# Performance work log

Hardware: AMD Instinct MI355X
Metric: run time of the kernel (lower is better)

Reference implementation:

```python
import jax, jax.numpy as jnp
import numpy as np

D_MODEL = 1024
N_HEADS = 16
MAX_SEQ = 1024
BATCH = 4

def _first_primes(n):
    limit = n * 15
    sieve = np.ones(limit, dtype=bool)
    sieve[:2] = False
    for i in range(2, int(limit ** 0.5) + 1):
        if sieve[i]:
            sieve[i * i::i] = False
    return np.flatnonzero(sieve)[:n]

def _pi_attention_bias(n_heads, max_seq_len):
    # bias[h, t, s] = 0.1 * sin(prime[h]*pi * (t - s) / max_seq_len)
    primes = _first_primes(n_heads).astype(np.float32)
    freqs = primes * np.pi  # [H]
    pos = np.arange(max_seq_len, dtype=np.float32)
    pos_diff = pos[:, None] - pos[None, :]  # [T, T]
    bias = np.sin(freqs[:, None, None] * pos_diff[None] / max_seq_len) * 0.1
    return jnp.asarray(bias, dtype=jnp.float32)

def setup_inputs() -> dict:
    key = jax.random.key(0)
    ks = jax.random.split(key, 8)
    D = D_MODEL
    xavier = (6.0 / (D + D)) ** 0.5
    inp = {
        'x': jax.random.normal(ks[0], (BATCH, MAX_SEQ, D), dtype=jnp.float32),
        'Wq': jax.random.uniform(ks[1], (D, D), jnp.float32, -xavier, xavier),
        'bq': jnp.zeros((D,), jnp.float32),
        'Wk': jax.random.uniform(ks[2], (D, D), jnp.float32, -xavier, xavier),
        'bk': jnp.zeros((D,), jnp.float32),
        'Wv': jax.random.uniform(ks[3], (D, D), jnp.float32, -xavier, xavier),
        'bv': jnp.zeros((D,), jnp.float32),
        'Wo': jax.random.uniform(ks[4], (D, D), jnp.float32, -xavier, xavier),
        'bo': jnp.zeros((D,), jnp.float32),
        'pi_bias': _pi_attention_bias(N_HEADS, MAX_SEQ),
        'bias_scale': jnp.asarray(0.1, jnp.float32),
        'spectral_alpha': jnp.asarray(1.0, jnp.float32),
    }
    return inp

def reference(x, Wq, bq, Wk, bk, Wv, bv, Wo, bo, pi_bias, bias_scale, spectral_alpha):
    B, T, D = x.shape
    H = N_HEADS
    hd = D // H
    scale = 1.0 / (hd ** 0.5)

    def split_heads(y):
        return y.reshape(B, T, H, hd).transpose(0, 2, 1, 3)  # [B,H,T,hd]

    q = split_heads(x @ Wq + bq)
    k = split_heads(x @ Wk + bk)
    v = split_heads(x @ Wv + bv)

    # spectral filter along the time axis (use_spectral and T > 4)
    freqs = jnp.fft.fftfreq(T).astype(jnp.float32)  # [T]
    filt = jnp.exp(-jnp.abs(spectral_alpha) * jnp.abs(freqs))[None, None, :, None]
    q = jnp.fft.ifft(jnp.fft.fft(q, axis=2, norm='ortho') * filt, axis=2, norm='ortho').real
    k = jnp.fft.ifft(jnp.fft.fft(k, axis=2, norm='ortho') * filt, axis=2, norm='ortho').real

    scores = jnp.einsum('bhtd,bhsd->bhts', q, k) * scale
    scores = scores + bias_scale * pi_bias[None, :, :T, :T]
    attn = jax.nn.softmax(scores, axis=-1)  # dropout is identity in eval
    out = jnp.einsum('bhts,bhsd->bhtd', attn, v)
    out = out.transpose(0, 2, 1, 3).reshape(B, T, D)
    return out @ Wo + bo
```

## Files before the change

kernel.cpp:

```cpp
#include <hip/hip_runtime.h>
#include <hip/hip_bf16.h>

typedef __bf16 bf16x8 __attribute__((ext_vector_type(8)));
typedef float f32x4 __attribute__((ext_vector_type(4)));

#define OFF_G      0x0ULL
#define OFF_GMAT   0x10000ULL
#define OFF_XB     0x210000ULL
#define OFF_XBT    0xA10000ULL
#define OFF_XF     0x1210000ULL
#define OFF_WQT    0x1A10000ULL
#define OFF_WKT    0x1C10000ULL
#define OFF_WVT    0x1E10000ULL
#define OFF_WOT    0x2010000ULL
#define OFF_KB     0x2210000ULL
#define OFF_VTB    0x2A10000ULL

static __device__ __forceinline__ unsigned short f2bf(float f) {
  union { float f; unsigned int u; } v; v.f = f;
  unsigned int r = v.u + 0x7FFFu + ((v.u >> 16) & 1u);
  return (unsigned short)(r >> 16);
}

static __device__ __forceinline__ void g2l16(const unsigned short* g, unsigned short* l) {
  __builtin_amdgcn_global_load_lds(
      (const __attribute__((address_space(1))) unsigned int*)g,
      (__attribute__((address_space(3))) unsigned int*)l, 16, 0, 0);
}

__constant__ float PRIMES_F[16] = {2.f, 3.f, 5.f, 7.f, 11.f, 13.f, 17.f, 19.f,
                                   23.f, 29.f, 31.f, 37.f, 41.f, 43.f, 47.f, 53.f};

__global__ __launch_bounds__(256) void k_g(const float* __restrict__ alpha_p,
                                           float* __restrict__ g) {
  const int d = blockIdx.x;
  const float alpha = fabsf(alpha_p[0]);
  float partial = 0.f;
  for (int j = threadIdx.x; j < 1024; j += 256) {
    int jm = (j <= 512) ? j : 1024 - j;
    float filt = __expf(-alpha * (float)jm * (1.0f / 1024.f));
    int p = (j * d) & 1023;
    partial += filt * __cosf((float)p * (6.28318530717958647692f / 1024.f));
  }
  __shared__ float red[4];
  #pragma unroll
  for (int off = 32; off > 0; off >>= 1) partial += __shfl_down(partial, off, 64);
  if ((threadIdx.x & 63) == 0) red[threadIdx.x >> 6] = partial;
  __syncthreads();
  if (threadIdx.x == 0) g[d] = (red[0] + red[1] + red[2] + red[3]) * (1.f / 1024.f);
}

__global__ __launch_bounds__(256) void k_gmat(const float* __restrict__ g,
                                              unsigned short* __restrict__ Gm) {
  int i = blockIdx.x * 256 + threadIdx.x;
  int t = i >> 10, s = i & 1023;
  Gm[i] = f2bf(g[(t - s) & 1023]);
}

__global__ __launch_bounds__(256) void k_prep(
    const float* __restrict__ x, const float* __restrict__ w0,
    const float* __restrict__ w1, const float* __restrict__ w2,
    const float* __restrict__ w3, unsigned short* __restrict__ xb,
    unsigned short* __restrict__ xbT, unsigned short* __restrict__ Wout) {
  __shared__ float tile[32][33];
  const int z = blockIdx.z;
  const bool isX = z < 4;
  const float* in = isX ? (x + ((long)z << 20))
                        : (z == 4 ? w0 : z == 5 ? w1 : z == 6 ? w2 : w3);
  const long ooff = isX ? ((long)z << 20) : ((long)(z - 4) << 20);
  const int r0 = blockIdx.y * 32, c0 = blockIdx.x * 32;
  const int tx = threadIdx.x & 31, ty = threadIdx.x >> 5;
  #pragma unroll
  for (int i = 0; i < 4; i++) {
    float v = in[(long)(r0 + ty + 8 * i) * 1024 + c0 + tx];
    tile[ty + 8 * i][tx] = v;
    if (isX) xb[ooff + (long)(r0 + ty + 8 * i) * 1024 + c0 + tx] = f2bf(v);
  }
  __syncthreads();
  unsigned short* outT = isX ? xbT : Wout;
  #pragma unroll
  for (int i = 0; i < 4; i++)
    outT[ooff + (long)(c0 + ty + 8 * i) * 1024 + r0 + tx] = f2bf(tile[tx][ty + 8 * i]);
}

#define GEMM_CORE(A_, Bt_, ACC_)                                                     \
  const int tid = threadIdx.x, l = tid & 63, wid = tid >> 6;                         \
  const int lr = l & 15, lg = l >> 4;                                                \
  const int wm = (wid >> 1) * 64, wn = (wid & 1) * 64;                               \
  const int srow = wid * 32 + (l >> 3);                                              \
  const int scol = ((l & 7) ^ (l >> 3)) * 8;                                         \
  const unsigned short* Ag = A_ + (long)(m0 + srow) * 1024 + scol;                   \
  const unsigned short* Bg = Bt_ + (long)(n0 + srow) * 1024 + scol;                  \
  unsigned short* Asw = As + wid * 32 * 64;                                          \
  unsigned short* Bsw = Bs + wid * 32 * 64;                                          \
  const int xk = (lr & 7) << 4;                                                      \
  const int co[2] = {(0 + lg * 16) ^ xk, (64 + lg * 16) ^ xk};                       \
  for (int kt = 0; kt < 1024; kt += 64) {                                            \
    __syncthreads();                                                                 \
    _Pragma("unroll")                                                                \
    for (int c = 0; c < 4; c++) {                                                    \
      g2l16(Ag + (long)c * 8 * 1024 + kt, Asw + c * 8 * 64);                         \
      g2l16(Bg + (long)c * 8 * 1024 + kt, Bsw + c * 8 * 64);                         \
    }                                                                                \
    __syncthreads();                                                                 \
    const char* Ab = (const char*)As;                                                \
    const char* Bb = (const char*)Bs;                                                \
    _Pragma("unroll")                                                                \
    for (int ks = 0; ks < 2; ks++) {                                                 \
      bf16x8 af[4], bfr[4];                                                          \
      _Pragma("unroll")                                                              \
      for (int mf = 0; mf < 4; mf++)                                                 \
        af[mf] = *(const bf16x8*)(Ab + (wm + mf * 16 + lr) * 128 + co[ks]);          \
      _Pragma("unroll")                                                              \
      for (int nf = 0; nf < 4; nf++)                                                 \
        bfr[nf] = *(const bf16x8*)(Bb + (wn + nf * 16 + lr) * 128 + co[ks]);         \
      _Pragma("unroll")                                                              \
      for (int mf = 0; mf < 4; mf++)                                                 \
        _Pragma("unroll")                                                            \
        for (int nf = 0; nf < 4; nf++)                                               \
          ACC_[mf][nf] = __builtin_amdgcn_mfma_f32_16x16x32_bf16(af[mf], bfr[nf],    \
                                                                 ACC_[mf][nf], 0, 0, 0); \
    }                                                                                \
  }

__global__ __launch_bounds__(256) void k_gemm5(
    const unsigned short* __restrict__ A, const unsigned short* __restrict__ Bt,
    const float* __restrict__ bias, const float* __restrict__ bias2,
    unsigned short* __restrict__ Cv, unsigned short* __restrict__ Cv2) {
  __shared__ __align__(16) unsigned short As[128 * 64];
  __shared__ __align__(16) unsigned short Bs[128 * 64];
  const int orig = (blockIdx.x & 7) * 64 + (blockIdx.x >> 3);
  const int m0 = (orig & 31) * 128, n0 = (orig >> 5) * 128;
  f32x4 acc[4][4] = {};
  GEMM_CORE(A, Bt, acc)
  #pragma unroll
  for (int nf = 0; nf < 4; nf++) {
    const int n = n0 + wn + nf * 16 + lr;
    const float bb = (n < 1024) ? bias[n] : bias2[n - 1024];
    unsigned short* Cd = (n < 1024) ? Cv : Cv2;
    #pragma unroll
    for (int mf = 0; mf < 4; mf++) {
      const int mb = m0 + wm + mf * 16 + lg * 4;
      #pragma unroll
      for (int r = 0; r < 4; r++)
        Cd[(long)(mb + r) * 1024 + (n & 1023)] = f2bf(acc[mf][nf][r] + bb);
    }
  }
}

__global__ __launch_bounds__(256) void k_fv(
    const unsigned short* __restrict__ Gm, const unsigned short* __restrict__ xbT,
    const unsigned short* __restrict__ WvT, const unsigned short* __restrict__ xb,
    const float* __restrict__ bv, unsigned short* __restrict__ Xf,
    unsigned short* __restrict__ Vtb) {
  __shared__ __align__(16) unsigned short As[128 * 64];
  __shared__ __align__(16) unsigned short Bs[128 * 64];
  const int orig = (blockIdx.x & 7) * 64 + (blockIdx.x >> 3);
  const bool isV = orig >= 256;
  const int o = isV ? orig - 256 : orig;
  const int m0 = (o & 7) * 128, n0 = (o >> 3) * 128;
  const unsigned short* A_ = isV ? WvT : Gm;
  const unsigned short* Bt_ = isV ? xb : xbT;
  f32x4 acc[4][4] = {};
  GEMM_CORE(A_, Bt_, acc)
  #pragma unroll
  for (int nf = 0; nf < 4; nf++) {
    const int n = n0 + wn + nf * 16 + lr;
    #pragma unroll
    for (int mf = 0; mf < 4; mf++) {
      const int mb = wm + mf * 16 + lg * 4;
      #pragma unroll
      for (int r = 0; r < 4; r++) {
        const int m = m0 + mb + r;
        float v = acc[mf][nf][r];
        if (isV) {
          Vtb[(long)m * 4096 + n] = f2bf(v + bv[m]);
        } else {
          Xf[(long)((n & ~1023) + m) * 1024 + (n & 1023)] = f2bf(v);
        }
      }
    }
  }
}

__global__ __launch_bounds__(256) void k_gemmO(
    const unsigned short* __restrict__ A, const unsigned short* __restrict__ Bt,
    const float* __restrict__ bias, float* __restrict__ C) {
  __shared__ __align__(16) unsigned short As[64 * 64];
  __shared__ __align__(16) unsigned short Bs[128 * 64];
  const int orig = (blockIdx.x & 7) * 64 + (blockIdx.x >> 3);
  const int m0 = (orig & 63) * 64, n0 = (orig >> 6) * 128;
  const int tid = threadIdx.x, l = tid & 63, wid = tid >> 6;
  const int lr = l & 15, lg = l >> 4;
  const int wm = (wid >> 1) * 32, wn = (wid & 1) * 64;
  const int scol = ((l & 7) ^ (l >> 3)) * 8;
  const unsigned short* Ag = A + (long)(m0 + wid * 16 + (l >> 3)) * 1024 + scol;
  const unsigned short* Bg = Bt + (long)(n0 + wid * 32 + (l >> 3)) * 1024 + scol;
  unsigned short* Asw = As + wid * 16 * 64;
  unsigned short* Bsw = Bs + wid * 32 * 64;
  const int xk = (lr & 7) << 4;
  const int co[2] = {(0 + lg * 16) ^ xk, (64 + lg * 16) ^ xk};
  f32x4 acc[2][4] = {};
  for (int kt = 0; kt < 1024; kt += 64) {
    __syncthreads();
    #pragma unroll
    for (int c = 0; c < 2; c++)
      g2l16(Ag + (long)c * 8 * 1024 + kt, Asw + c * 8 * 64);
    #pragma unroll
    for (int c = 0; c < 4; c++)
      g2l16(Bg + (long)c * 8 * 1024 + kt, Bsw + c * 8 * 64);
    __syncthreads();
    const char* Ab = (const char*)As;
    const char* Bb = (const char*)Bs;
    #pragma unroll
    for (int ks = 0; ks < 2; ks++) {
      bf16x8 af[2], bfr[4];
      #pragma unroll
      for (int mf = 0; mf < 2; mf++)
        af[mf] = *(const bf16x8*)(Ab + (wm + mf * 16 + lr) * 128 + co[ks]);
      #pragma unroll
      for (int nf = 0; nf < 4; nf++)
        bfr[nf] = *(const bf16x8*)(Bb + (wn + nf * 16 + lr) * 128 + co[ks]);
      #pragma unroll
      for (int mf = 0; mf < 2; mf++)
        #pragma unroll
        for (int nf = 0; nf < 4; nf++)
          acc[mf][nf] = __builtin_amdgcn_mfma_f32_16x16x32_bf16(af[mf], bfr[nf], acc[mf][nf], 0, 0, 0);
    }
  }
  #pragma unroll
  for (int nf = 0; nf < 4; nf++) {
    const int n = n0 + wn + nf * 16 + lr;
    const float bb = bias[n];
    #pragma unroll
    for (int mf = 0; mf < 2; mf++) {
      const int mb = m0 + wm + mf * 16 + lg * 4;
      #pragma unroll
      for (int r = 0; r < 4; r++)
        C[(long)(mb + r) * 1024 + n] = acc[mf][nf][r] + bb;
    }
  }
}

__global__ __launch_bounds__(512) void k_attn(
    const unsigned short* __restrict__ Qb, const unsigned short* __restrict__ Kb,
    const unsigned short* __restrict__ Vtb,
    const float* __restrict__ bias_scale_p, unsigned short* __restrict__ Ob) {
  __shared__ __align__(16) unsigned short Kbuf[2][64 * 64];
  __shared__ __align__(16) unsigned short Vbuf[2][64 * 64];
  __shared__ __align__(16) unsigned short Ps[8][16 * 64];
  const int bid = blockIdx.x;
  const int qt = (bid >> 3) & 7;
  const int hb = ((bid >> 6) << 3) | (bid & 7);
  const int h = hb & 15, b = hb >> 4;
  const int tid = threadIdx.x, l = tid & 63, wid = tid >> 6;
  const int lr = l & 15, lg = l >> 4;
  const int q0 = qt * 128;
  const float LOG2E = 1.44269504088896f;
  const float c10 = bias_scale_p[0] * 0.1f * LOG2E;
  const float k1 = 0.125f * LOG2E;
  const float fh = PRIMES_F[h] * 3.14159265358979323846f;
  const unsigned short* Vth = Vtb + (long)h * 64 * 4096 + b * 1024;
  const int xk = (lr & 7) << 4;
  const int co[2] = {(0 + lg * 16) ^ xk, (64 + lg * 16) ^ xk};
  const int scol = ((l & 7) ^ (l >> 3)) * 8;

  const unsigned short* kg = Kb + (long)(b * 1024 + wid * 8 + (l >> 3)) * 1024 + h * 64 + scol;
  const unsigned short* vg = Vth + (long)(wid * 8 + (l >> 3)) * 4096 + scol;
  unsigned short* kb0 = &Kbuf[0][wid * 8 * 64];
  unsigned short* kb1 = &Kbuf[1][wid * 8 * 64];
  unsigned short* vb0 = &Vbuf[0][wid * 8 * 64];
  unsigned short* vb1 = &Vbuf[1][wid * 8 * 64];
  #define STAGE_TO(KD, VD) \
    { g2l16(kg, KD); g2l16(vg, VD); kg += 64 * 1024; vg += 64; }

  STAGE_TO(kb0, vb0);

  bf16x8 af[2];
  #pragma unroll
  for (int ks = 0; ks < 2; ks++)
    af[ks] = *(const bf16x8*)(
        &Qb[(long)(b * 1024 + q0 + wid * 16 + lr) * 1024 + h * 64 + ks * 32 + lg * 8]);

  float st2[4], ct2[4];
  #pragma unroll
  for (int r = 0; r < 4; r++) {
    float tt = (float)(q0 + wid * 16 + lg * 4 + r);
    float s_, c_;
    __sincosf(fh * tt * (1.f / 1024.f), &s_, &c_);
    st2[r] = c10 * s_;
    ct2[r] = c10 * c_;
  }
  float ss4[4], cs4[4], sd, cd;
  __sincosf(fh * (1.f / 16.f), &sd, &cd);
  #pragma unroll
  for (int nf = 0; nf < 4; nf++)
    __sincosf(fh * (float)(nf * 16 + lr) * (1.f / 1024.f), &ss4[nf], &cs4[nf]);

  f32x4 acc_o[4] = {};
  float pden[4] = {};
  __syncthreads();

  for (int it = 0; it < 16; ++it) {
    const int cur = it & 1;
    if (it < 15) {
      if (cur) { STAGE_TO(kb0, vb0); } else { STAGE_TO(kb1, vb1); }
      asm volatile("s_waitcnt vmcnt(2)" ::: "memory");
    } else {
      asm volatile("s_waitcnt vmcnt(0)" ::: "memory");
    }
    __builtin_amdgcn_s_barrier();
    __builtin_amdgcn_sched_barrier(0);
    const char* Kbb = (const char*)&Kbuf[cur][0];
    const char* Vbb = (const char*)&Vbuf[cur][0];
    f32x4 accs[4] = {};
    #pragma unroll
    for (int ks = 0; ks < 2; ks++) {
      bf16x8 bfr[4];
      #pragma unroll
      for (int nf = 0; nf < 4; nf++)
        bfr[nf] = *(const bf16x8*)(Kbb + (nf * 16 + lr) * 128 + co[ks]);
      __builtin_amdgcn_s_setprio(1);
      #pragma unroll
      for (int nf = 0; nf < 4; nf++)
        accs[nf] = __builtin_amdgcn_mfma_f32_16x16x32_bf16(af[ks], bfr[nf], accs[nf], 0, 0, 0);
      __builtin_amdgcn_s_setprio(0);
    }
    char* Pw = (char*)&Ps[wid][0];
    #pragma unroll
    for (int nf = 0; nf < 4; nf++) {
      #pragma unroll
      for (int r = 0; r < 4; r++) {
        float v = fmaf(accs[nf][r], k1, fmaf(st2[r], cs4[nf], -ct2[r] * ss4[nf]));
        float p;
        asm("v_exp_f32 %0, %1" : "=v"(p) : "v"(v));
        pden[r] += p;
        union { float f; unsigned int u; } pu; pu.f = p;
        const int prow = lg * 4 + r;
        *(unsigned short*)(Pw + prow * 128 + ((nf * 32 + lr * 2) ^ ((prow & 7) << 4))) =
            (unsigned short)((pu.u + 0x8000u) >> 16);
      }
    }
    #pragma unroll
    for (int ks = 0; ks < 2; ks++) {
      bf16x8 pa = *(const bf16x8*)(Pw + lr * 128 + co[ks]);
      bf16x8 vb[4];
      #pragma unroll
      for (int nf = 0; nf < 4; nf++)
        vb[nf] = *(const bf16x8*)(Vbb + (nf * 16 + lr) * 128 + co[ks]);
      __builtin_amdgcn_s_setprio(1);
      #pragma unroll
      for (int nf = 0; nf < 4; nf++)
        acc_o[nf] = __builtin_amdgcn_mfma_f32_16x16x32_bf16(pa, vb[nf], acc_o[nf], 0, 0, 0);
      __builtin_amdgcn_s_setprio(0);
    }
    __builtin_amdgcn_sched_barrier(0);
    __builtin_amdgcn_s_barrier();
    #pragma unroll
    for (int nf = 0; nf < 4; nf++) {
      float c_ = cs4[nf] * cd - ss4[nf] * sd;
      ss4[nf] = ss4[nf] * cd + cs4[nf] * sd;
      cs4[nf] = c_;
    }
  }
  #undef STAGE_TO
  #pragma unroll
  for (int r = 0; r < 4; r++) {
    float dsum = pden[r];
    #pragma unroll
    for (int off = 1; off < 16; off <<= 1) dsum += __shfl_xor(dsum, off, 64);
    pden[r] = 1.0f / dsum;
  }
  const int tg = q0 + wid * 16 + lg * 4;
  #pragma unroll
  for (int nf = 0; nf < 4; nf++) {
    const int dd = nf * 16 + lr;
    #pragma unroll
    for (int r = 0; r < 4; r++) {
      float val = acc_o[nf][r] * pden[r];
      Ob[(long)(b * 1024 + tg + r) * 1024 + h * 64 + dd] = f2bf(val);
    }
  }
}

extern "C" void kernel_launch(void* const* d_in, const int* in_sizes, int n_in,
                              void* d_out, int out_size, void* d_ws, size_t ws_size,
                              hipStream_t stream) {
  const float* x   = (const float*)d_in[0];
  const float* Wq  = (const float*)d_in[1];
  const float* bq  = (const float*)d_in[2];
  const float* Wk  = (const float*)d_in[3];
  const float* bk  = (const float*)d_in[4];
  const float* Wv  = (const float*)d_in[5];
  const float* bv  = (const float*)d_in[6];
  const float* Wo  = (const float*)d_in[7];
  const float* bo  = (const float*)d_in[8];
  const float* bsc = (const float*)d_in[10];
  const float* alp = (const float*)d_in[11];
  char* ws = (char*)d_ws;
  float*          g   = (float*)(ws + OFF_G);
  unsigned short* Gm  = (unsigned short*)(ws + OFF_GMAT);
  unsigned short* xb  = (unsigned short*)(ws + OFF_XB);
  unsigned short* xbT = (unsigned short*)(ws + OFF_XBT);
  unsigned short* Xf  = (unsigned short*)(ws + OFF_XF);
  unsigned short* WqT = (unsigned short*)(ws + OFF_WQT);
  unsigned short* WvT = (unsigned short*)(ws + OFF_WVT);
  unsigned short* WoT = (unsigned short*)(ws + OFF_WOT);
  unsigned short* Qb  = xbT;
  unsigned short* Kb  = (unsigned short*)(ws + OFF_KB);
  unsigned short* Vtb = (unsigned short*)(ws + OFF_VTB);
  unsigned short* Ob  = Xf;

  k_g   <<<1024, 256, 0, stream>>>(alp, g);
  k_gmat<<<4096, 256, 0, stream>>>(g, Gm);
  k_prep<<<dim3(32, 32, 8), 256, 0, stream>>>(x, Wq, Wk, Wv, Wo, xb, xbT, WqT);
  k_fv<<<512, 256, 0, stream>>>(Gm, xbT, WvT, xb, bv, Xf, Vtb);
  k_gemm5<<<512, 256, 0, stream>>>(Xf, WqT, bq, bk, Qb, Kb);
  k_attn<<<512, 512, 0, stream>>>(Qb, Kb, Vtb, bsc, Ob);
  k_gemmO<<<512, 256, 0, stream>>>(Ob, WoT, bo, (float*)d_out);
}
```

Before: 123.2 us.

## Double-buffer GEMM LDS tiles and fold filter-kernel computation into prep launch

The GEMM kernels (k_gemm5, k_fv, k_gemmO) now keep two LDS buffers and prefetch the next K tile while MFMAs run on the current one. Partial vmcnt waits replace the two full __syncthreads per iteration. Separately, the k_g reduction is merged into k_prep as an extra z-slice, which removes one kernel launch. The cost is doubled LDS per block, which may lower occupancy, and correctness now rests on hand-written waitcnt counts.

```diff
diff --git a/kernel.cpp b/kernel.cpp
--- a/kernel.cpp
+++ b/kernel.cpp
@@ -31,25 +31,6 @@
 __constant__ float PRIMES_F[16] = {2.f, 3.f, 5.f, 7.f, 11.f, 13.f, 17.f, 19.f,
                                    23.f, 29.f, 31.f, 37.f, 41.f, 43.f, 47.f, 53.f};
 
-__global__ __launch_bounds__(256) void k_g(const float* __restrict__ alpha_p,
-                                           float* __restrict__ g) {
-  const int d = blockIdx.x;
-  const float alpha = fabsf(alpha_p[0]);
-  float partial = 0.f;
-  for (int j = threadIdx.x; j < 1024; j += 256) {
-    int jm = (j <= 512) ? j : 1024 - j;
-    float filt = __expf(-alpha * (float)jm * (1.0f / 1024.f));
-    int p = (j * d) & 1023;
-    partial += filt * __cosf((float)p * (6.28318530717958647692f / 1024.f));
-  }
-  __shared__ float red[4];
-  #pragma unroll
-  for (int off = 32; off > 0; off >>= 1) partial += __shfl_down(partial, off, 64);
-  if ((threadIdx.x & 63) == 0) red[threadIdx.x >> 6] = partial;
-  __syncthreads();
-  if (threadIdx.x == 0) g[d] = (red[0] + red[1] + red[2] + red[3]) * (1.f / 1024.f);
-}
-
 __global__ __launch_bounds__(256) void k_gmat(const float* __restrict__ g,
                                               unsigned short* __restrict__ Gm) {
   int i = blockIdx.x * 256 + threadIdx.x;
@@ -60,10 +41,29 @@
 __global__ __launch_bounds__(256) void k_prep(
     const float* __restrict__ x, const float* __restrict__ w0,
     const float* __restrict__ w1, const float* __restrict__ w2,
-    const float* __restrict__ w3, unsigned short* __restrict__ xb,
-    unsigned short* __restrict__ xbT, unsigned short* __restrict__ Wout) {
+    const float* __restrict__ w3, const float* __restrict__ alpha_p,
+    unsigned short* __restrict__ xb, unsigned short* __restrict__ xbT,
+    unsigned short* __restrict__ Wout, float* __restrict__ g) {
   __shared__ float tile[32][33];
+  __shared__ float red[4];
   const int z = blockIdx.z;
+  if (z == 8) {
+    const int d = blockIdx.y * 32 + blockIdx.x;
+    const float alpha = fabsf(alpha_p[0]);
+    float partial = 0.f;
+    for (int j = threadIdx.x; j < 1024; j += 256) {
+      int jm = (j <= 512) ? j : 1024 - j;
+      float filt = __expf(-alpha * (float)jm * (1.0f / 1024.f));
+      int p = (j * d) & 1023;
+      partial += filt * __cosf((float)p * (6.28318530717958647692f / 1024.f));
+    }
+    #pragma unroll
+    for (int off = 32; off > 0; off >>= 1) partial += __shfl_down(partial, off, 64);
+    if ((threadIdx.x & 63) == 0) red[threadIdx.x >> 6] = partial;
+    __syncthreads();
+    if (threadIdx.x == 0) g[d] = (red[0] + red[1] + red[2] + red[3]) * (1.f / 1024.f);
+    return;
+  }
   const bool isX = z < 4;
   const float* in = isX ? (x + ((long)z << 20))
                         : (z == 4 ? w0 : z == 5 ? w1 : z == 6 ? w2 : w3);
@@ -87,24 +87,38 @@
   const int tid = threadIdx.x, l = tid & 63, wid = tid >> 6;                         \
   const int lr = l & 15, lg = l >> 4;                                                \
   const int wm = (wid >> 1) * 64, wn = (wid & 1) * 64;                               \
-  const int srow = wid * 32 + (l >> 3);                                              \
   const int scol = ((l & 7) ^ (l >> 3)) * 8;                                         \
-  const unsigned short* Ag = A_ + (long)(m0 + srow) * 1024 + scol;                   \
-  const unsigned short* Bg = Bt_ + (long)(n0 + srow) * 1024 + scol;                  \
-  unsigned short* Asw = As + wid * 32 * 64;                                          \
-  unsigned short* Bsw = Bs + wid * 32 * 64;                                          \
+  const unsigned short* Ag = A_ + (long)(m0 + wid * 32 + (l >> 3)) * 1024 + scol;    \
+  const unsigned short* Bg = Bt_ + (long)(n0 + wid * 32 + (l >> 3)) * 1024 + scol;   \
   const int xk = (lr & 7) << 4;                                                      \
   const int co[2] = {(0 + lg * 16) ^ xk, (64 + lg * 16) ^ xk};                       \
-  for (int kt = 0; kt < 1024; kt += 64) {                                            \
-    __syncthreads();                                                                 \
+  {                                                                                  \
     _Pragma("unroll")                                                                \
     for (int c = 0; c < 4; c++) {                                                    \
-      g2l16(Ag + (long)c * 8 * 1024 + kt, Asw + c * 8 * 64);                         \
-      g2l16(Bg + (long)c * 8 * 1024 + kt, Bsw + c * 8 * 64);                         \
+      g2l16(Ag + (long)c * 8192, &As[0][wid * 2048 + c * 512]);                      \
+      g2l16(Bg + (long)c * 8192, &Bs[0][wid * 2048 + c * 512]);                      \
     }                                                                                \
-    __syncthreads();                                                                 \
-    const char* Ab = (const char*)As;                                                \
-    const char* Bb = (const char*)Bs;                                                \
+    Ag += 64; Bg += 64;                                                              \
+  }                                                                                  \
+  __syncthreads();                                               \
+  for (int t = 0; t < 16; ++t) {                                                     \
+    const int cur = t & 1;                                                           \
+    if (t < 15) {                                                                    \
+      const int nxt = cur ^ 1;                                                       \
+      _Pragma("unroll")                                                              \
+      for (int c = 0; c < 4; c++) {                                                  \
+        g2l16(Ag + (long)c * 8192, &As[nxt][wid * 2048 + c * 512]);                  \
+        g2l16(Bg + (long)c * 8192, &Bs[nxt][wid * 2048 + c * 512]);                  \
+      }                                                                              \
+      Ag += 64; Bg += 64;                                                            \
+      asm volatile("s_waitcnt vmcnt(8)" ::: "memory");    \
+    } else {                                                                         \
+      asm volatile("s_waitcnt vmcnt(0)" ::: "memory");                               \
+    }                                                                                \
+    __builtin_amdgcn_s_barrier();                                                    \
+    __builtin_amdgcn_sched_barrier(0);                                               \
+    const char* Ab = (const char*)&As[cur][0];                                       \
+    const char* Bb = (const char*)&Bs[cur][0];                                       \
     _Pragma("unroll")                                                                \
     for (int ks = 0; ks < 2; ks++) {                                                 \
       bf16x8 af[4], bfr[4];                                                          \
@@ -121,14 +135,16 @@
           ACC_[mf][nf] = __builtin_amdgcn_mfma_f32_16x16x32_bf16(af[mf], bfr[nf],    \
                                                                  ACC_[mf][nf], 0, 0, 0); \
     }                                                                                \
+    __builtin_amdgcn_sched_barrier(0);                                               \
+    __builtin_amdgcn_s_barrier();                                                    \
   }
 
 __global__ __launch_bounds__(256) void k_gemm5(
     const unsigned short* __restrict__ A, const unsigned short* __restrict__ Bt,
     const float* __restrict__ bias, const float* __restrict__ bias2,
     unsigned short* __restrict__ Cv, unsigned short* __restrict__ Cv2) {
-  __shared__ __align__(16) unsigned short As[128 * 64];
-  __shared__ __align__(16) unsigned short Bs[128 * 64];
+  __shared__ __align__(16) unsigned short As[2][128 * 64];
+  __shared__ __align__(16) unsigned short Bs[2][128 * 64];
   const int orig = (blockIdx.x & 7) * 64 + (blockIdx.x >> 3);
   const int m0 = (orig & 31) * 128, n0 = (orig >> 5) * 128;
   f32x4 acc[4][4] = {};
@@ -153,8 +169,8 @@
     const unsigned short* __restrict__ WvT, const unsigned short* __restrict__ xb,
     const float* __restrict__ bv, unsigned short* __restrict__ Xf,
     unsigned short* __restrict__ Vtb) {
-  __shared__ __align__(16) unsigned short As[128 * 64];
-  __shared__ __align__(16) unsigned short Bs[128 * 64];
+  __shared__ __align__(16) unsigned short As[2][128 * 64];
+  __shared__ __align__(16) unsigned short Bs[2][128 * 64];
   const int orig = (blockIdx.x & 7) * 64 + (blockIdx.x >> 3);
   const bool isV = orig >= 256;
   const int o = isV ? orig - 256 : orig;
@@ -186,8 +202,8 @@
 __global__ __launch_bounds__(256) void k_gemmO(
     const unsigned short* __restrict__ A, const unsigned short* __restrict__ Bt,
     const float* __restrict__ bias, float* __restrict__ C) {
-  __shared__ __align__(16) unsigned short As[64 * 64];
-  __shared__ __align__(16) unsigned short Bs[128 * 64];
+  __shared__ __align__(16) unsigned short As[2][64 * 64];
+  __shared__ __align__(16) unsigned short Bs[2][128 * 64];
   const int orig = (blockIdx.x & 7) * 64 + (blockIdx.x >> 3);
   const int m0 = (orig & 63) * 64, n0 = (orig >> 6) * 128;
   const int tid = threadIdx.x, l = tid & 63, wid = tid >> 6;
@@ -196,22 +212,34 @@
   const int scol = ((l & 7) ^ (l >> 3)) * 8;
   const unsigned short* Ag = A + (long)(m0 + wid * 16 + (l >> 3)) * 1024 + scol;
   const unsigned short* Bg = Bt + (long)(n0 + wid * 32 + (l >> 3)) * 1024 + scol;
-  unsigned short* Asw = As + wid * 16 * 64;
-  unsigned short* Bsw = Bs + wid * 32 * 64;
   const int xk = (lr & 7) << 4;
   const int co[2] = {(0 + lg * 16) ^ xk, (64 + lg * 16) ^ xk};
+  {
+    #pragma unroll
+    for (int c = 0; c < 2; c++) g2l16(Ag + (long)c * 8192, &As[0][wid * 1024 + c * 512]);
+    #pragma unroll
+    for (int c = 0; c < 4; c++) g2l16(Bg + (long)c * 8192, &Bs[0][wid * 2048 + c * 512]);
+    Ag += 64; Bg += 64;
+  }
+  __syncthreads();
   f32x4 acc[2][4] = {};
-  for (int kt = 0; kt < 1024; kt += 64) {
-    __syncthreads();
-    #pragma unroll
-    for (int c = 0; c < 2; c++)
-      g2l16(Ag + (long)c * 8 * 1024 + kt, Asw + c * 8 * 64);
-    #pragma unroll
-    for (int c = 0; c < 4; c++)
-      g2l16(Bg + (long)c * 8 * 1024 + kt, Bsw + c * 8 * 64);
-    __syncthreads();
-    const char* Ab = (const char*)As;
-    const char* Bb = (const char*)Bs;
+  for (int t = 0; t < 16; ++t) {
+    const int cur = t & 1;
+    if (t < 15) {
+      const int nxt = cur ^ 1;
+      #pragma unroll
+      for (int c = 0; c < 2; c++) g2l16(Ag + (long)c * 8192, &As[nxt][wid * 1024 + c * 512]);
+      #pragma unroll
+      for (int c = 0; c < 4; c++) g2l16(Bg + (long)c * 8192, &Bs[nxt][wid * 2048 + c * 512]);
+      Ag += 64; Bg += 64;
+      asm volatile("s_waitcnt vmcnt(6)" ::: "memory");
+    } else {
+      asm volatile("s_waitcnt vmcnt(0)" ::: "memory");
+    }
+    __builtin_amdgcn_s_barrier();
+    __builtin_amdgcn_sched_barrier(0);
+    const char* Ab = (const char*)&As[cur][0];
+    const char* Bb = (const char*)&Bs[cur][0];
     #pragma unroll
     for (int ks = 0; ks < 2; ks++) {
       bf16x8 af[2], bfr[4];
@@ -227,6 +255,8 @@
         for (int nf = 0; nf < 4; nf++)
           acc[mf][nf] = __builtin_amdgcn_mfma_f32_16x16x32_bf16(af[mf], bfr[nf], acc[mf][nf], 0, 0, 0);
     }
+    __builtin_amdgcn_sched_barrier(0);
+    __builtin_amdgcn_s_barrier();
   }
   #pragma unroll
   for (int nf = 0; nf < 4; nf++) {
@@ -411,9 +441,8 @@
   unsigned short* Vtb = (unsigned short*)(ws + OFF_VTB);
   unsigned short* Ob  = Xf;
 
-  k_g   <<<1024, 256, 0, stream>>>(alp, g);
+  k_prep<<<dim3(32, 32, 9), 256, 0, stream>>>(x, Wq, Wk, Wv, Wo, alp, xb, xbT, WqT, g);
   k_gmat<<<4096, 256, 0, stream>>>(g, Gm);
-  k_prep<<<dim3(32, 32, 8), 256, 0, stream>>>(x, Wq, Wk, Wv, Wo, xb, xbT, WqT);
   k_fv<<<512, 256, 0, stream>>>(Gm, xbT, WvT, xb, bv, Xf, Vtb);
   k_gemm5<<<512, 256, 0, stream>>>(Xf, WqT, bq, bk, Qb, Kb);
   k_attn<<<512, 512, 0, stream>>>(Qb, Kb, Vtb, bsc, Ob);
```

Measured after the change: 122.6 us. Within noise of the previous version (-0.5%).
